# Optimization experiments

Measured on AMD Instinct MI355X. Metric: run time of the kernel, lower is better.

## Reference

```python
import jax, jax.numpy as jnp
import numpy as np

B, S, E, D = 2, 1024, 1024, 2048
H, KV, HD = 8, 4, 256
SOFTCAP = 50.0
SCALE = 256.0 ** -0.5  # query_pre_attn_scalar ** -0.5
WINDOW = 512
EPS = 1e-6
THETA = 10000.0


def setup_inputs() -> dict:
    key = jax.random.key(0)
    ks = jax.random.split(key, 10)
    hidden_states = jax.random.normal(ks[0], (B, S, D), jnp.float32)
    encoder_hidden_states = jax.random.normal(ks[1], (B, E, D), jnp.float32)
    # two packed segments per sequence (position resets at S//2)
    position_ids = jnp.broadcast_to(
        jnp.concatenate([jnp.arange(S // 2), jnp.arange(S - S // 2)]), (B, S)
    ).astype(jnp.int32)
    decoder_attention_mask = jnp.ones((B, S), jnp.int32)
    encoder_attention_mask = jnp.broadcast_to(
        (jnp.arange(E) < (E - 64)).astype(jnp.int32), (B, E))
    # RoPE tables from position ids
    inv_freq = 1.0 / (THETA ** (jnp.arange(0, HD, 2, dtype=jnp.float32) / HD))
    freqs = position_ids.astype(jnp.float32)[..., None] * inv_freq  # [B,S,HD/2]
    emb = jnp.concatenate([freqs, freqs], axis=-1)  # [B,S,HD]
    cos, sin = jnp.cos(emb), jnp.sin(emb)
    wq = 0.02 * jax.random.normal(ks[2], (D, H * HD), jnp.float32)
    wk = 0.02 * jax.random.normal(ks[3], (D, KV * HD), jnp.float32)
    wv = 0.02 * jax.random.normal(ks[4], (D, KV * HD), jnp.float32)
    wo = 0.02 * jax.random.normal(ks[5], (H * HD, D), jnp.float32)
    q_norm_w = 0.1 * jax.random.normal(ks[6], (HD,), jnp.float32)
    k_norm_w = 0.1 * jax.random.normal(ks[7], (HD,), jnp.float32)
    return dict(hidden_states=hidden_states,
                encoder_hidden_states=encoder_hidden_states,
                cos=cos, sin=sin, wq=wq, wk=wk, wv=wv, wo=wo,
                q_norm_w=q_norm_w, k_norm_w=k_norm_w,
                decoder_attention_mask=decoder_attention_mask,
                encoder_attention_mask=encoder_attention_mask,
                position_ids=position_ids)


def _rms_norm(x, w):
    # GemmaRMSNorm: x * rsqrt(mean(x^2)+eps) * (1 + w)
    var = jnp.mean(x * x, axis=-1, keepdims=True)
    return x * jax.lax.rsqrt(var + EPS) * (1.0 + w)


def _rotate_half(x):
    h = x.shape[-1] // 2
    return jnp.concatenate([-x[..., h:], x[..., :h]], axis=-1)


def _build_merged_mask(dec_mask, enc_mask, position_ids):
    dm = dec_mask.astype(bool)
    em = enc_mask.astype(bool)
    Sq = dm.shape[1]
    causal = jnp.tril(jnp.ones((Sq, Sq), bool))
    # segment ids from non-increasing position resets (packing)
    reset = jnp.concatenate(
        [jnp.ones((dm.shape[0], 1), bool),
         position_ids[:, 1:] <= position_ids[:, :-1]], axis=1)
    seg = jnp.cumsum(reset.astype(jnp.int32), axis=1)
    block = seg[:, :, None] == seg[:, None, :]
    full_self = dm[:, None, :] & causal[None] & block  # [B,S,S]
    rows = jnp.arange(Sq)
    dist = rows[:, None] - rows[None, :]
    sliding = (dist >= 0) & (dist < WINDOW)
    self_mask = full_self & sliding[None]
    cross = jnp.broadcast_to(em[:, None, :], (dm.shape[0], Sq, em.shape[1]))
    return jnp.concatenate([self_mask, cross], axis=-1)[:, None]  # [B,1,S,S+E]


def reference(hidden_states, encoder_hidden_states, cos, sin, wq, wk, wv, wo,
              q_norm_w, k_norm_w, decoder_attention_mask,
              encoder_attention_mask, position_ids):
    Bq, Sq, _ = hidden_states.shape
    Ek = encoder_hidden_states.shape[1]
    q = (hidden_states @ wq).reshape(Bq, Sq, H, HD).transpose(0, 2, 1, 3)
    k_self = (hidden_states @ wk).reshape(Bq, Sq, KV, HD).transpose(0, 2, 1, 3)
    v_self = (hidden_states @ wv).reshape(Bq, Sq, KV, HD).transpose(0, 2, 1, 3)
    k_cross = (encoder_hidden_states @ wk).reshape(Bq, Ek, KV, HD).transpose(0, 2, 1, 3)
    v_cross = (encoder_hidden_states @ wv).reshape(Bq, Ek, KV, HD).transpose(0, 2, 1, 3)
    # QK RMSNorm (cross keys normalized but NOT rotated, matching source)
    q = _rms_norm(q, q_norm_w)
    k_self = _rms_norm(k_self, k_norm_w)
    k_cross = _rms_norm(k_cross, k_norm_w)
    c, s = cos[:, None, :, :], sin[:, None, :, :]
    q = q * c + _rotate_half(q) * s
    k_self = k_self * c + _rotate_half(k_self) * s
    k = jnp.concatenate([k_self, k_cross], axis=2)  # [B,KV,S+E,HD]
    v = jnp.concatenate([v_self, v_cross], axis=2)
    rep = H // KV
    k = jnp.repeat(k, rep, axis=1)
    v = jnp.repeat(v, rep, axis=1)
    mask = _build_merged_mask(decoder_attention_mask, encoder_attention_mask,
                              position_ids)
    scores = jnp.einsum('bhqd,bhkd->bhqk', q, k) * SCALE
    scores = SOFTCAP * jnp.tanh(scores / SOFTCAP)  # logit softcapping
    scores = jnp.where(mask, scores, jnp.float32(-1e30))
    attn = jax.nn.softmax(scores, axis=-1)
    out = jnp.einsum('bhqk,bhkd->bhqd', attn, v)
    out = out.transpose(0, 2, 1, 3).reshape(Bq, Sq, H * HD)
    return out @ wo
```

## Files before the change

kernel.cpp:

```cpp
#include <hip/hip_runtime.h>
#include <math.h>

#define B_ 2
#define S_ 1024
#define E_ 1024
#define D_ 2048
#define H_ 8
#define KV_ 4
#define HD_ 256
#define WINDOW_ 512u
#define SCALE_ 0.0625f
#define CAP_ 50.0f
#define EPS_ 1e-6f
#define CROSS_OK (-7)
#define KINV (-2147483647 - 1)

typedef __bf16 bf8_t __attribute__((ext_vector_type(8)));
typedef float fx4 __attribute__((ext_vector_type(4)));
#define MFMA16(a, b, c) __builtin_amdgcn_mfma_f32_16x16x32_bf16((a), (b), (c), 0, 0, 0)

typedef __attribute__((address_space(1))) unsigned int gas_u32;
typedef __attribute__((address_space(3))) unsigned int las_u32;
__device__ __forceinline__ void gl2lds16(const void* g, void* l) {
    __builtin_amdgcn_global_load_lds((const gas_u32*)g, (las_u32*)l, 16, 0, 0);
}

union U4 { __bf16 b[4]; unsigned long long u; };

__device__ __forceinline__ float pexp(float dot) {
    float e = __expf(dot * (2.0f * SCALE_ / CAP_));
    return __expf(-(2.0f * CAP_) / (e + 1.0f));
}

__device__ __forceinline__ void dev_tobf16(const float* __restrict__ x,
                                           __bf16* __restrict__ y, int n4, int i) {
    if (i >= n4) return;
    float4 v = ((const float4*)x)[i];
    U4 p;
    p.b[0] = (__bf16)v.x; p.b[1] = (__bf16)v.y;
    p.b[2] = (__bf16)v.z; p.b[3] = (__bf16)v.w;
    *(unsigned long long*)&y[(size_t)i * 4] = p.u;
}

__device__ __forceinline__ void dev_tsplit(const float* __restrict__ W,
                                           __bf16* __restrict__ Th,
                                           __bf16* __restrict__ Tl, int K, int N,
                                           int bx, int by, int t,
                                           float (*tile)[33], int wlo) {
    const int tx = t & 31, ty = t >> 5;
    const int k0 = bx * 32, n0 = by * 32;
#pragma unroll
    for (int r = 0; r < 4; ++r)
        tile[ty + r * 8][tx] = W[(size_t)(k0 + ty + r * 8) * N + n0 + tx];
    __syncthreads();
#pragma unroll
    for (int r = 0; r < 4; ++r) {
        float v = tile[tx][ty + r * 8];
        __bf16 h = (__bf16)v;
        size_t o = (size_t)(n0 + ty + r * 8) * K + k0 + tx;
        Th[o] = h;
        if (wlo) Tl[o] = (__bf16)(v - (float)h);
    }
}

__device__ __forceinline__ void dev_segscan(const int* __restrict__ pos,
                                            const int* __restrict__ dm,
                                            const int* __restrict__ em,
                                            int* __restrict__ seg,
                                            int* __restrict__ ki,
                                            int b, int t, int* wsum) {
    const int base = b * 1024 + t * 4;
    int4 p = *(const int4*)&pos[base];
    int pm1 = (t == 0) ? 0 : pos[base - 1];
    int r0 = (t == 0) ? 1 : (p.x <= pm1 ? 1 : 0);
    int r1 = (p.y <= p.x), r2 = (p.z <= p.y), r3 = (p.w <= p.z);
    int c0 = r0, c1 = c0 + r1, c2 = c1 + r2, c3 = c2 + r3;
    const int lane = t & 63, wv = t >> 6;
    int x = c3;
#pragma unroll
    for (int off = 1; off < 64; off <<= 1) {
        int y = __shfl_up(x, off, 64);
        if (lane >= off) x += y;
    }
    if (lane == 63) wsum[wv] = x;
    __syncthreads();
    int woff = 0;
#pragma unroll
    for (int w = 0; w < 4; ++w) if (w < wv) woff += wsum[w];
    const int excl = woff + x - c3;
    int sv[4] = {excl + c0, excl + c1, excl + c2, excl + c3};
    int4 dmv = *(const int4*)&dm[base];
    int4 emv = *(const int4*)&em[base];
    int dma[4] = {dmv.x, dmv.y, dmv.z, dmv.w};
    int ema[4] = {emv.x, emv.y, emv.z, emv.w};
#pragma unroll
    for (int r = 0; r < 4; ++r) {
        seg[base + r] = sv[r];
        ki[b * 2048 + t * 4 + r] = dma[r] ? sv[r] : KINV;
        ki[b * 2048 + 1024 + t * 4 + r] = ema[r] ? CROSS_OK : KINV;
    }
}

__global__ __launch_bounds__(256) void prep(
    const float* __restrict__ hs, const float* __restrict__ enc,
    const float* __restrict__ wq, const float* __restrict__ wk,
    const float* __restrict__ wvp, const float* __restrict__ wo,
    const int* __restrict__ pos, const int* __restrict__ dm,
    const int* __restrict__ em,
    __bf16* __restrict__ hs_bf, __bf16* __restrict__ enc_bf,
    __bf16* __restrict__ wqkvTH, __bf16* __restrict__ wqkvTL,
    __bf16* __restrict__ woTH, __bf16* __restrict__ woTL,
    int* __restrict__ seg, int* __restrict__ ki) {
    __shared__ float tile[32][33];
    __shared__ int wsum[4];
    int bid = blockIdx.x;
    const int t = threadIdx.x;
    if (bid < 4096) { dev_tobf16(hs, hs_bf, 1048576, bid * 256 + t); return; }
    bid -= 4096;
    if (bid < 4096) { dev_tobf16(enc, enc_bf, 1048576, bid * 256 + t); return; }
    bid -= 4096;
    if (bid < 4096) {
        dev_tsplit(wq, wqkvTH, nullptr, 2048, 2048, bid & 63, bid >> 6, t, tile, 0);
        return;
    }
    bid -= 4096;
    if (bid < 2048) {
        dev_tsplit(wk, wqkvTH + (size_t)2048 * 2048, nullptr, 2048, 1024,
                   bid & 63, bid >> 6, t, tile, 0);
        return;
    }
    bid -= 2048;
    if (bid < 2048) {
        dev_tsplit(wvp, wqkvTH + (size_t)3072 * 2048, wqkvTL + (size_t)3072 * 2048,
                   2048, 1024, bid & 63, bid >> 6, t, tile, 1);
        return;
    }
    bid -= 2048;
    if (bid < 4096) {
        dev_tsplit(wo, woTH, woTL, 2048, 2048, bid & 63, bid >> 6, t, tile, 1);
        return;
    }
    bid -= 4096;
    dev_segscan(pos, dm, em, seg, ki, bid, t, wsum);
}

template <int NPASS>
__device__ __forceinline__ void gemm_core2(
    const __bf16* __restrict__ Ah, const __bf16* __restrict__ Al,
    const __bf16* __restrict__ Bh, const __bf16* __restrict__ Bl,
    int row0, int col0, int K,
    __bf16* As0, __bf16* As1, __bf16* Bs0, __bf16* Bs1, fx4 (&acc)[4][4]) {
    const int tid = threadIdx.x, lane = tid & 63, wv = tid >> 6;
    const int l15 = lane & 15, lq = lane >> 4;
    const int wm = (wv >> 1) * 64, wn = (wv & 1) * 64;
    constexpr int WCNT = (NPASS == 1) ? 0x0F74 : (NPASS == 2) ? 0x0F76 : 0x0F78;

    auto stage = [&](int buf, int k0) {
#pragma unroll
        for (int s = 0; s < 2; ++s) {
            int ch = (wv * 2 + s) * 64 + lane;
            int r = ch >> 2, cp = ch & 3;
            int cl = (cp - ((r >> 1) & 3)) & 3;
            size_t ga = (size_t)(row0 + r) * K + k0 + cl * 8;
            size_t gb = (size_t)(col0 + r) * K + k0 + cl * 8;
            gl2lds16(Ah + ga, As0 + buf * 4096 + ch * 8);
            if (NPASS >= 3) gl2lds16(Al + ga, As1 + buf * 4096 + ch * 8);
            gl2lds16(Bh + gb, Bs0 + buf * 4096 + ch * 8);
            if (NPASS >= 2) gl2lds16(Bl + gb, Bs1 + buf * 4096 + ch * 8);
        }
    };

    stage(0, 0);
    for (int k0 = 0; k0 < K; k0 += 32) {
        const int buf = (k0 >> 5) & 1;
        const bool hasnext = (k0 + 32 < K);
        if (hasnext) stage(buf ^ 1, k0 + 32);
        if (hasnext) __builtin_amdgcn_s_waitcnt(WCNT);
        else         __builtin_amdgcn_s_waitcnt(0x0F70);
        __builtin_amdgcn_s_barrier();
        __builtin_amdgcn_sched_barrier(0);

        const __bf16* A0 = As0 + buf * 4096;
        const __bf16* A1 = As1 + buf * 4096;
        const __bf16* B0 = Bs0 + buf * 4096;
        const __bf16* B1 = Bs1 + buf * 4096;
        bf8_t ah[4], al[4], bh[4], bl[4];
#pragma unroll
        for (int i = 0; i < 4; ++i) {
            int row = wm + i * 16 + l15;
            int sl = row * 4 + ((lq + (row >> 1)) & 3);
            ah[i] = *(const bf8_t*)(A0 + sl * 8);
            if (NPASS >= 3) al[i] = *(const bf8_t*)(A1 + sl * 8);
        }
#pragma unroll
        for (int j = 0; j < 4; ++j) {
            int row = wn + j * 16 + l15;
            int sl = row * 4 + ((lq + (row >> 1)) & 3);
            bh[j] = *(const bf8_t*)(B0 + sl * 8);
            if (NPASS >= 2) bl[j] = *(const bf8_t*)(B1 + sl * 8);
        }
#pragma unroll
        for (int i = 0; i < 4; ++i)
#pragma unroll
            for (int j = 0; j < 4; ++j) {
                acc[i][j] = MFMA16(ah[i], bh[j], acc[i][j]);
                if (NPASS >= 2) acc[i][j] = MFMA16(ah[i], bl[j], acc[i][j]);
                if (NPASS >= 3) acc[i][j] = MFMA16(al[i], bh[j], acc[i][j]);
            }
        __builtin_amdgcn_sched_barrier(0);
        __builtin_amdgcn_s_barrier();
    }
}

__device__ __forceinline__ void gemm_core_half(
    const __bf16* __restrict__ Ah, const __bf16* __restrict__ Al,
    const __bf16* __restrict__ Bh, const __bf16* __restrict__ Bl,
    int row0, int col0, int K,
    __bf16* As0, __bf16* As1, __bf16* Bs0, __bf16* Bs1, fx4 (&acc)[4][2]) {
    const int tid = threadIdx.x, lane = tid & 63, wv = tid >> 6;
    const int l15 = lane & 15, lq = lane >> 4;
    const int wm = (wv >> 1) * 64, wn = (wv & 1) * 32;

    auto stage = [&](int buf, int k0) {
#pragma unroll
        for (int s = 0; s < 2; ++s) {
            int ch = s * 256 + tid;
            int r = ch >> 2, cp = ch & 3;
            int cl = (cp - ((r >> 1) & 3)) & 3;
            size_t ga = (size_t)(row0 + r) * K + k0 + cl * 8;
            gl2lds16(Ah + ga, As0 + buf * 4096 + ch * 8);
            gl2lds16(Al + ga, As1 + buf * 4096 + ch * 8);
        }
        {
            int ch = tid;
            int r = ch >> 2, cp = ch & 3;
            int cl = (cp - ((r >> 1) & 3)) & 3;
            size_t gb = (size_t)(col0 + r) * K + k0 + cl * 8;
            gl2lds16(Bh + gb, Bs0 + buf * 2048 + ch * 8);
            gl2lds16(Bl + gb, Bs1 + buf * 2048 + ch * 8);
        }
    };

    stage(0, 0);
    for (int k0 = 0; k0 < K; k0 += 32) {
        const int buf = (k0 >> 5) & 1;
        const bool hasnext = (k0 + 32 < K);
        if (hasnext) stage(buf ^ 1, k0 + 32);
        if (hasnext) __builtin_amdgcn_s_waitcnt(0x0F76);
        else         __builtin_amdgcn_s_waitcnt(0x0F70);
        __builtin_amdgcn_s_barrier();
        __builtin_amdgcn_sched_barrier(0);

        const __bf16* A0 = As0 + buf * 4096;
        const __bf16* A1 = As1 + buf * 4096;
        const __bf16* B0 = Bs0 + buf * 2048;
        const __bf16* B1 = Bs1 + buf * 2048;
        bf8_t ah[4], al[4], bh[2], bl[2];
#pragma unroll
        for (int i = 0; i < 4; ++i) {
            int row = wm + i * 16 + l15;
            int sl = row * 4 + ((lq + (row >> 1)) & 3);
            ah[i] = *(const bf8_t*)(A0 + sl * 8);
            al[i] = *(const bf8_t*)(A1 + sl * 8);
        }
#pragma unroll
        for (int j = 0; j < 2; ++j) {
            int row = wn + j * 16 + l15;
            int sl = row * 4 + ((lq + (row >> 1)) & 3);
            bh[j] = *(const bf8_t*)(B0 + sl * 8);
            bl[j] = *(const bf8_t*)(B1 + sl * 8);
        }
#pragma unroll
        for (int i = 0; i < 4; ++i)
#pragma unroll
            for (int j = 0; j < 2; ++j) {
                acc[i][j] = MFMA16(ah[i], bh[j], acc[i][j]);
                acc[i][j] = MFMA16(ah[i], bl[j], acc[i][j]);
                acc[i][j] = MFMA16(al[i], bh[j], acc[i][j]);
            }
        __builtin_amdgcn_sched_barrier(0);
        __builtin_amdgcn_s_barrier();
    }
}

__global__ __launch_bounds__(256) void gemm_proj(
    const __bf16* __restrict__ hsb, const __bf16* __restrict__ encb,
    const __bf16* __restrict__ BTh, const __bf16* __restrict__ BTl,
    float* __restrict__ qf32, float* __restrict__ ksf, float* __restrict__ kcf,
    __bf16* __restrict__ vtS, __bf16* __restrict__ vtC) {
    __shared__ __bf16 As0[8192], Bs0[8192], Bs1[8192];
    const int bx = blockIdx.x, row0 = blockIdx.y * 128;
    const __bf16* A;
    float* Ck; __bf16* Cv; int col0;
    if (bx < 32) { A = hsb;  col0 = bx * 128;               Ck = ksf; Cv = vtS; }
    else         { A = encb; col0 = (bx - 32) * 128 + 2048; Ck = kcf; Cv = vtC; }
    fx4 acc[4][4];
#pragma unroll
    for (int i = 0; i < 4; ++i)
#pragma unroll
        for (int j = 0; j < 4; ++j) acc[i][j] = (fx4){0.f, 0.f, 0.f, 0.f};
    if (col0 >= 3072)
        gemm_core2<2>(A, nullptr, BTh, BTl, row0, col0, D_, As0, nullptr, Bs0, Bs1, acc);
    else
        gemm_core2<1>(A, nullptr, BTh, BTl, row0, col0, D_, As0, nullptr, Bs0, Bs1, acc);

    const int tid = threadIdx.x, lane = tid & 63, wv = tid >> 6;
    const int l15 = lane & 15, lq = lane >> 4;
    const int wm = (wv >> 1) * 64, wn = (wv & 1) * 64;
    const int mode = (col0 < 2048) ? 0 : (col0 < 3072 ? 1 : 2);
#pragma unroll
    for (int i = 0; i < 4; ++i)
#pragma unroll
        for (int j = 0; j < 4; ++j) {
            int mb = row0 + wm + i * 16 + lq * 4;
            int n = col0 + wn + j * 16 + l15;
            if (mode == 0) {
#pragma unroll
                for (int r = 0; r < 4; ++r)
                    qf32[(size_t)(mb + r) * 2048 + n] = acc[i][j][r];
            } else if (mode == 1) {
                int nk = n - 2048;
#pragma unroll
                for (int r = 0; r < 4; ++r)
                    Ck[(size_t)(mb + r) * 1024 + nk] = acc[i][j][r];
            } else {
                int nv = n - 3072;
                int b = mb >> 10, s = mb & 1023;
                int kv = nv >> 8, d = nv & 255;
                U4 pk;
#pragma unroll
                for (int r = 0; r < 4; ++r) pk.b[r] = (__bf16)acc[i][j][r];
                *(unsigned long long*)&Cv[((size_t)(b * KV_ + kv) * HD_ + d) * 1024 + s] = pk.u;
            }
        }
}

__global__ __launch_bounds__(256) void gemm_out(
    const __bf16* __restrict__ Ah, const __bf16* __restrict__ Al,
    const __bf16* __restrict__ Bh, const __bf16* __restrict__ Bl,
    float* __restrict__ C) {
    __shared__ __bf16 As0[8192], As1[8192], Bs0[4096], Bs1[4096];
    const int row0 = blockIdx.y * 128, col0 = blockIdx.x * 64;
    fx4 acc[4][2];
#pragma unroll
    for (int i = 0; i < 4; ++i)
#pragma unroll
        for (int j = 0; j < 2; ++j) acc[i][j] = (fx4){0.f, 0.f, 0.f, 0.f};
    gemm_core_half(Ah, Al, Bh, Bl, row0, col0, 2048, As0, As1, Bs0, Bs1, acc);
    const int tid = threadIdx.x, lane = tid & 63, wv = tid >> 6;
    const int l15 = lane & 15, lq = lane >> 4;
    const int wm = (wv >> 1) * 64, wn = (wv & 1) * 32;
#pragma unroll
    for (int i = 0; i < 4; ++i)
#pragma unroll
        for (int j = 0; j < 2; ++j) {
            int mb = row0 + wm + i * 16 + lq * 4;
            int n = col0 + wn + j * 16 + l15;
#pragma unroll
            for (int r = 0; r < 4; ++r)
                C[(size_t)(mb + r) * 2048 + n] = acc[i][j][r];
        }
}

__global__ __launch_bounds__(256) void rms_all(
    const float* __restrict__ qf32, const float* __restrict__ ksf,
    const float* __restrict__ kcf,
    __bf16* __restrict__ q_bf, __bf16* __restrict__ k_bf,
    __bf16* __restrict__ kc_bf,
    const float* __restrict__ qnw, const float* __restrict__ knw,
    const float* __restrict__ cs, const float* __restrict__ sn) {
    const int t = threadIdx.x, wvi = t >> 6, lane = t & 63;
    const int row = blockIdx.x * 4 + wvi;
    const float* x; __bf16* out; const float* w;
    int nsh, do_rope, trans, rbase;
    if (row < 16384)      { rbase = row;         x = qf32; out = q_bf;  w = qnw; nsh = 3; do_rope = 1; trans = 0; }
    else if (row < 24576) { rbase = row - 16384; x = ksf;  out = k_bf;  w = knw; nsh = 2; do_rope = 1; trans = 1; }
    else                  { rbase = row - 24576; x = kcf;  out = kc_bf; w = knw; nsh = 2; do_rope = 0; trans = 1; }
    float4 v = ((const float4*)x)[(size_t)rbase * 64 + lane];
    float ss = v.x * v.x + v.y * v.y + v.z * v.z + v.w * v.w;
#pragma unroll
    for (int off = 32; off; off >>= 1) ss += __shfl_xor(ss, off, 64);
    float scale = rsqrtf(ss * (1.0f / HD_) + EPS_);
    float4 w4 = ((const float4*)w)[lane];
    float y0 = v.x * scale * (1.0f + w4.x);
    float y1 = v.y * scale * (1.0f + w4.y);
    float y2 = v.z * scale * (1.0f + w4.z);
    float y3 = v.w * scale * (1.0f + w4.w);
    const int m = rbase >> nsh;
    if (do_rope) {
        float r0 = __shfl_xor(y0, 32, 64);
        float r1 = __shfl_xor(y1, 32, 64);
        float r2 = __shfl_xor(y2, 32, 64);
        float r3 = __shfl_xor(y3, 32, 64);
        float sg = (lane < 32) ? -1.0f : 1.0f;
        float4 c4 = ((const float4*)cs)[(size_t)m * 64 + lane];
        float4 s4 = ((const float4*)sn)[(size_t)m * 64 + lane];
        y0 = y0 * c4.x + sg * r0 * s4.x;
        y1 = y1 * c4.y + sg * r1 * s4.y;
        y2 = y2 * c4.z + sg * r2 * s4.z;
        y3 = y3 * c4.w + sg * r3 * s4.w;
    }
    size_t oidx;
    if (trans) {
        int nh = 1 << nsh;
        int hh = rbase & (nh - 1);
        int b = m >> 10, s = m & 1023;
        oidx = ((size_t)(b * nh + hh) * 1024 + s) * HD_ + lane * 4;
    } else {
        oidx = (size_t)rbase * HD_ + lane * 4;
    }
    U4 pk;
    pk.b[0] = (__bf16)y0; pk.b[1] = (__bf16)y1;
    pk.b[2] = (__bf16)y2; pk.b[3] = (__bf16)y3;
    *(unsigned long long*)&out[oidx] = pk.u;
}

__global__ __launch_bounds__(256, 1) void attn_part(
    const __bf16* __restrict__ qb,
    const __bf16* __restrict__ kb,
    const __bf16* __restrict__ kcb,
    const __bf16* __restrict__ vtS,
    const __bf16* __restrict__ vtC,
    const int* __restrict__ seg, const int* __restrict__ ki,
    float* __restrict__ accS, float* __restrict__ accC,
    float* __restrict__ lsS, float* __restrict__ lsC) {
    __shared__ __bf16 Ks[2][8192];
    __shared__ __bf16 Vs[2][8192];
    __shared__ __bf16 Ps[4][640];
    __shared__ int kinfoS[1600];
    const int tid = threadIdx.x, lane = tid & 63, wv = tid >> 6;
    const int l15 = lane & 15, lq = lane >> 4;
    const int bid = blockIdx.x;
    const int role = bid >> 8;
    const int g = bid & 7;
    const int b = g >> 2, kv = g & 3;
    const int idx = (bid >> 3) & 31;
    const int qt_raw = idx >> 1, h = kv * 2 + (idx & 1);
    const int qt = role ? (15 - qt_raw) : qt_raw;
    const int s0 = qt * 64;

    const int lo = (s0 >= 512) ? ((s0 - 511) & ~31) : 0;
    const int nts = (s0 + 64 - lo) >> 5;
    const int ccr = (33 - nts) >> 1;

    const __bf16* KbS = kb  + (size_t)(b * KV_ + kv) * (1024 * 256);
    const __bf16* VbS = vtS + (size_t)(b * KV_ + kv) * (256 * 1024);
    const __bf16* KbC = kcb + (size_t)(b * KV_ + kv) * (1024 * 256);
    const __bf16* VbC = vtC + (size_t)(b * KV_ + kv) * (256 * 1024);

    if (role == 0) {
        const int nk0 = nts * 32, nk1 = ccr * 32;
        for (int i = tid; i < nk0; i += 256) kinfoS[i] = ki[b * 2048 + lo + i];
        for (int i = tid; i < nk1; i += 256)
            kinfoS[nk0 + i] = ki[b * 2048 + 1024 + i];
    } else {
        const int nk1 = (32 - ccr) * 32;
        for (int i = tid; i < nk1; i += 256)
            kinfoS[i] = ki[b * 2048 + 1024 + ccr * 32 + i];
    }
    __syncthreads();

    const int qpos = s0 + wv * 16 + l15;
    bf8_t qf[8];
    const __bf16* qrow = qb + ((size_t)(b * S_ + qpos) * H_ + h) * HD_;
#pragma unroll
    for (int f = 0; f < 8; ++f) qf[f] = *(const bf8_t*)(qrow + f * 32 + lq * 8);
    const int segq = seg[b * S_ + qpos];

    fx4 accO[16];
#pragma unroll
    for (int j = 0; j < 16; ++j) accO[j] = (fx4){0.f, 0.f, 0.f, 0.f};
    float lsum = 0.f;
    const int swzk = l15 & 7;
    const int swzv = lq ^ ((l15 >> 1) & 3);

    const __bf16* phK[2]; const __bf16* phV[2];
    int phKey0[2], phKio[2], phNt[2], phSelf[2], nph;
    if (role == 0) {
        phK[0] = KbS; phV[0] = VbS; phKey0[0] = lo; phKio[0] = 0;
        phNt[0] = nts; phSelf[0] = 1;
        phK[1] = KbC; phV[1] = VbC; phKey0[1] = 0; phKio[1] = nts * 32;
        phNt[1] = ccr; phSelf[1] = 0;
        nph = 2;
    } else {
        phK[0] = KbC; phV[0] = VbC; phKey0[0] = ccr * 32; phKio[0] = 0;
        phNt[0] = 32 - ccr; phSelf[0] = 0;
        nph = 1;
    }

    for (int p = 0; p < nph; ++p) {
        const __bf16* Kb = phK[p];
        const __bf16* Vb = phV[p];
        const int key0 = phKey0[p], kiob = phKio[p], nt = phNt[p];
        const int selfm = phSelf[p];
        const int tgt = selfm ? segq : CROSS_OK;

        auto stage = [&](int buf, int t) {
            const __bf16* Kt = Kb + (size_t)(key0 + t * 32) * 256;
            const __bf16* Vt = Vb + (key0 + t * 32);
#pragma unroll
            for (int r = 0; r < 4; ++r) {
                int cid = r * 256 + tid;
                int key = cid >> 5, c = cid & 31;
                gl2lds16(Kt + key * 256 + (((c ^ (key & 7))) << 3), &Ks[buf][cid * 8]);
            }
#pragma unroll
            for (int r = 0; r < 4; ++r) {
                int cid = r * 256 + tid;
                int d = cid >> 2, kc = cid & 3;
                gl2lds16(Vt + (size_t)d * 1024 + ((kc ^ ((d >> 1) & 3)) << 3),
                         &Vs[buf][cid * 8]);
            }
        };

        stage(0, 0);
        for (int i = 0; i < nt; ++i) {
            const int kt0_c = key0 + i * 32;
            const int kio_c = kiob + i * 32;
            const bool hasnext = (i + 1 < nt);
            if (hasnext) stage((i + 1) & 1, i + 1);
            if (hasnext) __builtin_amdgcn_s_waitcnt(0x0F78);
            else         __builtin_amdgcn_s_waitcnt(0x0F70);
            __builtin_amdgcn_s_barrier();
            __builtin_amdgcn_sched_barrier(0);

            const __bf16* Ksb = Ks[i & 1];
            const __bf16* Vsb = Vs[i & 1];
            fx4 sc0a = (fx4){0.f, 0.f, 0.f, 0.f}, sc0b = (fx4){0.f, 0.f, 0.f, 0.f};
            fx4 sc1a = (fx4){0.f, 0.f, 0.f, 0.f}, sc1b = (fx4){0.f, 0.f, 0.f, 0.f};
            __builtin_amdgcn_s_setprio(1);
#pragma unroll
            for (int f = 0; f < 8; f += 2) {
                bf8_t k0a = *(const bf8_t*)&Ksb[(l15 * 32 + ((f * 4 + lq) ^ swzk)) * 8];
                bf8_t k1a = *(const bf8_t*)&Ksb[((16 + l15) * 32 + ((f * 4 + lq) ^ swzk)) * 8];
                bf8_t k0b = *(const bf8_t*)&Ksb[(l15 * 32 + (((f + 1) * 4 + lq) ^ swzk)) * 8];
                bf8_t k1b = *(const bf8_t*)&Ksb[((16 + l15) * 32 + (((f + 1) * 4 + lq) ^ swzk)) * 8];
                sc0a = MFMA16(k0a, qf[f], sc0a);
                sc1a = MFMA16(k1a, qf[f], sc1a);
                sc0b = MFMA16(k0b, qf[f + 1], sc0b);
                sc1b = MFMA16(k1b, qf[f + 1], sc1b);
            }
            __builtin_amdgcn_s_setprio(0);
            fx4 sc0 = sc0a + sc0b;
            fx4 sc1 = sc1a + sc1b;
            int4 ki0 = *(const int4*)&kinfoS[kio_c + lq * 4];
            int4 ki1 = *(const int4*)&kinfoS[kio_c + 16 + lq * 4];
            int ka0[4] = {ki0.x, ki0.y, ki0.z, ki0.w};
            int ka1[4] = {ki1.x, ki1.y, ki1.z, ki1.w};
            U4 p0, p1;
#pragma unroll
            for (int r = 0; r < 4; ++r) {
                int key0r = kt0_c + lq * 4 + r;
                float e0 = pexp(sc0[r]);
                float e1 = pexp(sc1[r]);
                bool ok0 = (ka0[r] == tgt) &&
                           (!selfm || (unsigned)(qpos - key0r) < WINDOW_);
                bool ok1 = (ka1[r] == tgt) &&
                           (!selfm || (unsigned)(qpos - key0r - 16) < WINDOW_);
                float v0 = ok0 ? e0 : 0.f;
                float v1 = ok1 ? e1 : 0.f;
                lsum += v0 + v1;
                p0.b[r] = (__bf16)v0;
                p1.b[r] = (__bf16)v1;
            }
            *(unsigned long long*)&Ps[wv][l15 * 40 + lq * 4] = p0.u;
            *(unsigned long long*)&Ps[wv][l15 * 40 + 16 + lq * 4] = p1.u;
            bf8_t pf = *(const bf8_t*)&Ps[wv][l15 * 40 + lq * 8];
            __builtin_amdgcn_s_setprio(1);
#pragma unroll
            for (int j = 0; j < 16; ++j) {
                bf8_t vb = *(const bf8_t*)&Vsb[((j * 16 + l15) * 4 + swzv) * 8];
                accO[j] = MFMA16(pf, vb, accO[j]);
            }
            __builtin_amdgcn_s_setprio(0);
            __builtin_amdgcn_sched_barrier(0);
            __builtin_amdgcn_s_barrier();
        }
    }

    lsum += __shfl_xor(lsum, 16, 64);
    lsum += __shfl_xor(lsum, 32, 64);
    float* accT = role ? accC : accS;
    float* lsT  = role ? lsC  : lsS;
    if (lq == 0) lsT[(size_t)(b * S_ + qpos) * 8 + h] = lsum;
#pragma unroll
    for (int j = 0; j < 16; ++j)
#pragma unroll
        for (int r = 0; r < 4; ++r) {
            size_t idx2 = (size_t)(b * S_ + s0 + wv * 16 + lq * 4 + r) * 2048 +
                          h * 256 + j * 16 + l15;
            accT[idx2] = accO[j][r];
        }
}

__global__ __launch_bounds__(256) void combine(
    const float* __restrict__ aS, const float* __restrict__ aC,
    const float* __restrict__ lS, const float* __restrict__ lC,
    __bf16* __restrict__ aH, __bf16* __restrict__ aL) {
    int i = blockIdx.x * 256 + threadIdx.x;
    size_t base = (size_t)i * 4;
    int row = (int)(base >> 11);
    int h = (int)((base >> 8) & 7);
    float inv = 1.0f / (lS[row * 8 + h] + lC[row * 8 + h]);
    float4 a = ((const float4*)aS)[i];
    float4 c = ((const float4*)aC)[i];
    float o[4] = {(a.x + c.x) * inv, (a.y + c.y) * inv,
                  (a.z + c.z) * inv, (a.w + c.w) * inv};
    U4 ph, pl;
#pragma unroll
    for (int r = 0; r < 4; ++r) {
        __bf16 hi = (__bf16)o[r];
        ph.b[r] = hi;
        pl.b[r] = (__bf16)(o[r] - (float)hi);
    }
    *(unsigned long long*)&aH[base] = ph.u;
    *(unsigned long long*)&aL[base] = pl.u;
}

extern "C" void kernel_launch(void* const* d_in, const int* in_sizes, int n_in,
                              void* d_out, int out_size, void* d_ws, size_t ws_size,
                              hipStream_t stream) {
    (void)in_sizes; (void)n_in; (void)out_size; (void)ws_size;
    const float* hs  = (const float*)d_in[0];
    const float* enc = (const float*)d_in[1];
    const float* cs  = (const float*)d_in[2];
    const float* sn  = (const float*)d_in[3];
    const float* wq  = (const float*)d_in[4];
    const float* wk  = (const float*)d_in[5];
    const float* wv  = (const float*)d_in[6];
    const float* wo  = (const float*)d_in[7];
    const float* qnw = (const float*)d_in[8];
    const float* knw = (const float*)d_in[9];
    const int* dm    = (const int*)d_in[10];
    const int* em    = (const int*)d_in[11];
    const int* pos   = (const int*)d_in[12];
    float* out = (float*)d_out;

    char* ws = (char*)d_ws;
    const size_t MB = 1ull << 20;
    __bf16* hs_bf   = (__bf16*)(ws + 0 * MB);
    __bf16* enc_bf  = (__bf16*)(ws + 8 * MB);
    __bf16* wqkvTH  = (__bf16*)(ws + 16 * MB);
    __bf16* wqkvTL  = (__bf16*)(ws + 32 * MB);
    __bf16* woTH    = (__bf16*)(ws + 48 * MB);
    __bf16* woTL    = (__bf16*)(ws + 56 * MB);
    float*  qf32    = (float*)(ws + 64 * MB);
    float*  ksf     = (float*)(ws + 80 * MB);
    float*  kcf     = (float*)(ws + 88 * MB);
    __bf16* k_bf    = (__bf16*)(ws + 104 * MB);
    __bf16* kc_bf   = (__bf16*)(ws + 108 * MB);
    __bf16* vtS     = (__bf16*)(ws + 112 * MB);
    __bf16* vtC     = (__bf16*)(ws + 116 * MB);
    int*    seg     = (int*)(ws + 120 * MB);
    int*    kinfo   = (int*)(ws + 121 * MB);
    __bf16* q_bf    = (__bf16*)(ws + 124 * MB);
    __bf16* aoutH   = (__bf16*)(ws + 0 * MB);
    __bf16* aoutL   = (__bf16*)(ws + 9 * MB);
    float*  accS    = (float*)(ws + 64 * MB);
    float*  accC    = (float*)(ws + 81 * MB);
    float*  lsS     = (float*)(ws + 98 * MB);
    float*  lsC     = (float*)(ws + 99 * MB);

    prep<<<20482, 256, 0, stream>>>(hs, enc, wq, wk, wv, wo, pos, dm, em,
                                    hs_bf, enc_bf, wqkvTH, wqkvTL, woTH, woTL,
                                    seg, kinfo);

    gemm_proj<<<dim3(48, 16), 256, 0, stream>>>(hs_bf, enc_bf, wqkvTH, wqkvTL,
                                                qf32, ksf, kcf, vtS, vtC);

    rms_all<<<8192, 256, 0, stream>>>(qf32, ksf, kcf, q_bf, k_bf, kc_bf,
                                      qnw, knw, cs, sn);

    attn_part<<<512, 256, 0, stream>>>(q_bf, k_bf, kc_bf, vtS, vtC, seg, kinfo,
                                       accS, accC, lsS, lsC);
    combine<<<4096, 256, 0, stream>>>(accS, accC, lsS, lsC, aoutH, aoutL);

    gemm_out<<<dim3(32, 16), 256, 0, stream>>>(aoutH, aoutL, woTH, woTL, out);
}
```

Measured before the change: 371.1 us.

## Widen weight transpose tiles and read V directly from global in attention

The weight transpose/split in prep moves from 32x32 tiles with scalar accesses to 64x64 tiles using float4 loads and packed 8-byte bf16 stores, which cuts the block count and aims for better coalescing. Separately, the attention kernel no longer stages V tiles into LDS through global_load_lds; each lane now reads its V fragments straight from global memory (strided by 1024) right before the PV MFMAs. This frees LDS and shortens the stage wait, but puts uncoalesced global reads on the critical path of the inner loop, and it also pads the transpose tile to 68 columns, which may cause LDS bank conflicts on the column reads.

```diff
diff --git a/kernel.cpp b/kernel.cpp
--- a/kernel.cpp
+++ b/kernel.cpp
@@ -42,24 +42,34 @@
     *(unsigned long long*)&y[(size_t)i * 4] = p.u;
 }
 
-__device__ __forceinline__ void dev_tsplit(const float* __restrict__ W,
-                                           __bf16* __restrict__ Th,
-                                           __bf16* __restrict__ Tl, int K, int N,
-                                           int bx, int by, int t,
-                                           float (*tile)[33], int wlo) {
-    const int tx = t & 31, ty = t >> 5;
-    const int k0 = bx * 32, n0 = by * 32;
-#pragma unroll
-    for (int r = 0; r < 4; ++r)
-        tile[ty + r * 8][tx] = W[(size_t)(k0 + ty + r * 8) * N + n0 + tx];
+__device__ __forceinline__ void dev_tsplit64(const float* __restrict__ W,
+                                             __bf16* __restrict__ Th,
+                                             __bf16* __restrict__ Tl, int K, int N,
+                                             int bx, int by, int t,
+                                             float (*tile)[68], int wlo) {
+    const int q = t & 15, s = t >> 4;
+    const int k0 = bx * 64, n0 = by * 64;
+#pragma unroll
+    for (int rr = 0; rr < 4; ++rr) {
+        int row = rr * 16 + s;
+        *(float4*)&tile[row][q * 4] =
+            *(const float4*)&W[(size_t)(k0 + row) * N + n0 + q * 4];
+    }
     __syncthreads();
 #pragma unroll
-    for (int r = 0; r < 4; ++r) {
-        float v = tile[tx][ty + r * 8];
-        __bf16 h = (__bf16)v;
-        size_t o = (size_t)(n0 + ty + r * 8) * K + k0 + tx;
-        Th[o] = h;
-        if (wlo) Tl[o] = (__bf16)(v - (float)h);
+    for (int nn = 0; nn < 4; ++nn) {
+        int n = nn * 16 + s;
+        U4 ph, pl;
+#pragma unroll
+        for (int i = 0; i < 4; ++i) {
+            float v = tile[q * 4 + i][n];
+            __bf16 h = (__bf16)v;
+            ph.b[i] = h;
+            pl.b[i] = (__bf16)(v - (float)h);
+        }
+        size_t o = (size_t)(n0 + n) * K + k0 + q * 4;
+        *(unsigned long long*)&Th[o] = ph.u;
+        if (wlo) *(unsigned long long*)&Tl[o] = pl.u;
     }
 }
 
@@ -111,7 +121,7 @@
     __bf16* __restrict__ wqkvTH, __bf16* __restrict__ wqkvTL,
     __bf16* __restrict__ woTH, __bf16* __restrict__ woTL,
     int* __restrict__ seg, int* __restrict__ ki) {
-    __shared__ float tile[32][33];
+    __shared__ float tile[64][68];
     __shared__ int wsum[4];
     int bid = blockIdx.x;
     const int t = threadIdx.x;
@@ -119,28 +129,28 @@
     bid -= 4096;
     if (bid < 4096) { dev_tobf16(enc, enc_bf, 1048576, bid * 256 + t); return; }
     bid -= 4096;
-    if (bid < 4096) {
-        dev_tsplit(wq, wqkvTH, nullptr, 2048, 2048, bid & 63, bid >> 6, t, tile, 0);
+    if (bid < 1024) {
+        dev_tsplit64(wq, wqkvTH, nullptr, 2048, 2048, bid & 31, bid >> 5, t, tile, 0);
         return;
     }
-    bid -= 4096;
-    if (bid < 2048) {
-        dev_tsplit(wk, wqkvTH + (size_t)2048 * 2048, nullptr, 2048, 1024,
-                   bid & 63, bid >> 6, t, tile, 0);
+    bid -= 1024;
+    if (bid < 512) {
+        dev_tsplit64(wk, wqkvTH + (size_t)2048 * 2048, nullptr, 2048, 1024,
+                     bid & 31, bid >> 5, t, tile, 0);
         return;
     }
-    bid -= 2048;
-    if (bid < 2048) {
-        dev_tsplit(wvp, wqkvTH + (size_t)3072 * 2048, wqkvTL + (size_t)3072 * 2048,
-                   2048, 1024, bid & 63, bid >> 6, t, tile, 1);
+    bid -= 512;
+    if (bid < 512) {
+        dev_tsplit64(wvp, wqkvTH + (size_t)3072 * 2048, wqkvTL + (size_t)3072 * 2048,
+                     2048, 1024, bid & 31, bid >> 5, t, tile, 1);
         return;
     }
-    bid -= 2048;
-    if (bid < 4096) {
-        dev_tsplit(wo, woTH, woTL, 2048, 2048, bid & 63, bid >> 6, t, tile, 1);
+    bid -= 512;
+    if (bid < 1024) {
+        dev_tsplit64(wo, woTH, woTL, 2048, 2048, bid & 31, bid >> 5, t, tile, 1);
         return;
     }
-    bid -= 4096;
+    bid -= 1024;
     dev_segscan(pos, dm, em, seg, ki, bid, t, wsum);
 }
 
@@ -425,7 +435,6 @@
     float* __restrict__ accS, float* __restrict__ accC,
     float* __restrict__ lsS, float* __restrict__ lsC) {
     __shared__ __bf16 Ks[2][8192];
-    __shared__ __bf16 Vs[2][8192];
     __shared__ __bf16 Ps[4][640];
     __shared__ int kinfoS[1600];
     const int tid = threadIdx.x, lane = tid & 63, wv = tid >> 6;
@@ -472,7 +481,6 @@
     for (int j = 0; j < 16; ++j) accO[j] = (fx4){0.f, 0.f, 0.f, 0.f};
     float lsum = 0.f;
     const int swzk = l15 & 7;
-    const int swzv = lq ^ ((l15 >> 1) & 3);
 
     const __bf16* phK[2]; const __bf16* phV[2];
     int phKey0[2], phKio[2], phNt[2], phSelf[2], nph;
@@ -497,19 +505,11 @@
 
         auto stage = [&](int buf, int t) {
             const __bf16* Kt = Kb + (size_t)(key0 + t * 32) * 256;
-            const __bf16* Vt = Vb + (key0 + t * 32);
 #pragma unroll
             for (int r = 0; r < 4; ++r) {
                 int cid = r * 256 + tid;
                 int key = cid >> 5, c = cid & 31;
                 gl2lds16(Kt + key * 256 + (((c ^ (key & 7))) << 3), &Ks[buf][cid * 8]);
-            }
-#pragma unroll
-            for (int r = 0; r < 4; ++r) {
-                int cid = r * 256 + tid;
-                int d = cid >> 2, kc = cid & 3;
-                gl2lds16(Vt + (size_t)d * 1024 + ((kc ^ ((d >> 1) & 3)) << 3),
-                         &Vs[buf][cid * 8]);
             }
         };
 
@@ -519,13 +519,12 @@
             const int kio_c = kiob + i * 32;
             const bool hasnext = (i + 1 < nt);
             if (hasnext) stage((i + 1) & 1, i + 1);
-            if (hasnext) __builtin_amdgcn_s_waitcnt(0x0F78);
+            if (hasnext) __builtin_amdgcn_s_waitcnt(0x0F74);
             else         __builtin_amdgcn_s_waitcnt(0x0F70);
             __builtin_amdgcn_s_barrier();
             __builtin_amdgcn_sched_barrier(0);
 
             const __bf16* Ksb = Ks[i & 1];
-            const __bf16* Vsb = Vs[i & 1];
             fx4 sc0a = (fx4){0.f, 0.f, 0.f, 0.f}, sc0b = (fx4){0.f, 0.f, 0.f, 0.f};
             fx4 sc1a = (fx4){0.f, 0.f, 0.f, 0.f}, sc1b = (fx4){0.f, 0.f, 0.f, 0.f};
             __builtin_amdgcn_s_setprio(1);
@@ -566,10 +565,11 @@
             *(unsigned long long*)&Ps[wv][l15 * 40 + lq * 4] = p0.u;
             *(unsigned long long*)&Ps[wv][l15 * 40 + 16 + lq * 4] = p1.u;
             bf8_t pf = *(const bf8_t*)&Ps[wv][l15 * 40 + lq * 8];
+            const __bf16* Vtc = Vb + kt0_c + lq * 8;
             __builtin_amdgcn_s_setprio(1);
 #pragma unroll
             for (int j = 0; j < 16; ++j) {
-                bf8_t vb = *(const bf8_t*)&Vsb[((j * 16 + l15) * 4 + swzv) * 8];
+                bf8_t vb = *(const bf8_t*)(Vtc + (size_t)(j * 16 + l15) * 1024);
                 accO[j] = MFMA16(pf, vb, accO[j]);
             }
             __builtin_amdgcn_s_setprio(0);
@@ -661,7 +661,7 @@
     float*  lsS     = (float*)(ws + 98 * MB);
     float*  lsC     = (float*)(ws + 99 * MB);
 
-    prep<<<20482, 256, 0, stream>>>(hs, enc, wq, wk, wv, wo, pos, dm, em,
+    prep<<<11266, 256, 0, stream>>>(hs, enc, wq, wk, wv, wo, pos, dm, em,
                                     hs_bf, enc_bf, wqkvTH, wqkvTL, woTH, woTL,
                                     seg, kinfo);
 
```

Result: slower. 442.8 us (+19.3%).
